# Optimization experiments

Measured on AMD Instinct MI355X. Metric: run time of the kernel, lower is better.

The kernel has to match this reference:

```python
import jax, jax.numpy as jnp
import numpy as np
import itertools

# The repo's eset_ops_4_to_4 builds 69 permutation-equivariant basis ops on a
# rank-4 set tensor x[n, d, i, j, k, l]. We reconstruct the 69-dim basis as all
# order-preserving subset matchings (A, B) with A = kept input index slots,
# B = output slots receiving them (|A| = |B| = s, s = 1..4): sum x over the
# complement of A, then broadcast the reduced tensor into output positions B.
# Count: sum_{s=1..4} C(4,s)^2 = 16 + 36 + 16 + 1 = 69 (Vandermonde C(8,4)=70
# minus the s=0 global-sum term).

def _basis_pairs():
    pairs = []
    for s in range(1, 5):
        for A in itertools.combinations(range(4), s):
            for B in itertools.combinations(range(4), s):
                pairs.append((A, B))
    return pairs  # len == 69

_PAIRS = _basis_pairs()


def _forward(x, coefs, bias):
    # x: (n, d, N, N, N, N); coefs: (d, s_out, 69); bias: (1, s_out, 1,1,1,1)
    out_shape = (x.shape[0], coefs.shape[1]) + x.shape[2:]
    out = jnp.zeros(out_shape, x.dtype)
    for idx, (A, B) in enumerate(_PAIRS):
        sum_axes = tuple(2 + i for i in range(4) if i not in A)
        red = x.sum(axis=sum_axes) if sum_axes else x  # (n, d, N^|A|)
        # mix channels on the SMALL reduced tensor (op and channel mix commute)
        term = jnp.einsum('ds,nd...->ns...', coefs[:, :, idx], red)
        # place kept axes at output slots B (order-preserving), broadcast rest
        for p in range(4):
            if p not in B:
                term = jnp.expand_dims(term, axis=2 + p)
        out = out + term  # broadcasting add == broadcast then accumulate
    return out + bias


def setup_inputs() -> dict:
    key = jax.random.key(0)
    k1, k2 = jax.random.split(key)
    n, d, s_out, N, basis = 2, 8, 8, 32, 69
    x = jax.random.normal(k1, (n, d, N, N, N, N), dtype=jnp.float32)
    std = np.sqrt(2.0 / (d + s_out + basis)).astype(np.float32)
    coefs = std * jax.random.normal(k2, (d, s_out, basis), dtype=jnp.float32)
    bias = jnp.zeros((1, s_out, 1, 1, 1, 1), dtype=jnp.float32)
    return {'x': x, 'coefs': coefs, 'bias': bias}


def reference(x, coefs, bias):
    return _forward(x, coefs, bias)
```

## Files before the change

kernel.cpp:

```cpp
#include <hip/hip_runtime.h>


constexpr size_t R3SZ  = 524288;
constexpr size_t R2SZ  = 16384;
constexpr size_t R1SZ  = 512;
constexpr size_t R3OFF = 0;
constexpr size_t R2OFF = R3OFF + 4 * R3SZ;
constexpr size_t R1OFF = R2OFF + 6 * R2SZ;
constexpr size_t T2OFF = R1OFF + 4 * R1SZ;
constexpr size_t T1OFF = T2OFF + 6 * R2SZ;
constexpr size_t U3OFF = T1OFF + 4 * R1SZ;

__global__ __launch_bounds__(512) void k_red3(const float* __restrict__ x,
                                              float* __restrict__ ws) {
    __shared__ float4 cp[32][4][8];
    __shared__ float  b012[1024];
    __shared__ float4 a2[256];
    const int bid  = blockIdx.x;
    const int t    = threadIdx.x;
    const int half = t >> 8;
    const int tt   = t & 255;
    const int k    = tt >> 3;
    const int l4   = tt & 7;

    if (bid < 512) {
        const int i    = bid & 31;
        const int nd   = bid >> 5;
        const int w4   = (t >> 6) & 3;
        const int lane = t & 63;
        const float* xp = x + ((size_t)nd << 20) + ((size_t)i << 15) + k * 32 + l4 * 4;
        float4 acc = {0.f, 0.f, 0.f, 0.f};
        #pragma unroll
        for (int it = 0; it < 16; ++it) {
            const int j = it * 2 + half;
            float4 v = *(const float4*)(xp + j * 1024);
            acc.x += v.x; acc.y += v.y; acc.z += v.z; acc.w += v.w;
            float h = v.x + v.y + v.z + v.w;
            h += __shfl_xor(h, 1); h += __shfl_xor(h, 2); h += __shfl_xor(h, 4);
            if (l4 == 0) b012[j * 32 + k] = h;
            v.x += __shfl_xor(v.x, 8);  v.y += __shfl_xor(v.y, 8);
            v.z += __shfl_xor(v.z, 8);  v.w += __shfl_xor(v.w, 8);
            v.x += __shfl_xor(v.x, 16); v.y += __shfl_xor(v.y, 16);
            v.z += __shfl_xor(v.z, 16); v.w += __shfl_xor(v.w, 16);
            v.x += __shfl_xor(v.x, 32); v.y += __shfl_xor(v.y, 32);
            v.z += __shfl_xor(v.z, 32); v.w += __shfl_xor(v.w, 32);
            if (lane < 8) cp[j][w4][lane] = v;
        }
        if (half == 1) a2[tt] = acc;
        __syncthreads();
        const size_t base = ((size_t)nd << 15) + ((size_t)i << 10);
        *(float2*)(ws + R3OFF + base + 2 * t) = *(const float2*)(b012 + 2 * t);
        if (half == 0) {
            const int j = tt >> 3, lj = tt & 7;
            float4 s0 = cp[j][0][lj], s1 = cp[j][1][lj];
            float4 s2 = cp[j][2][lj], s3 = cp[j][3][lj];
            float4 s;
            s.x = s0.x + s1.x + s2.x + s3.x;
            s.y = s0.y + s1.y + s2.y + s3.y;
            s.z = s0.z + s1.z + s2.z + s3.z;
            s.w = s0.w + s1.w + s2.w + s3.w;
            *(float4*)(ws + R3OFF + R3SZ + base + j * 32 + lj * 4) = s;
            float4 b = a2[tt];
            acc.x += b.x; acc.y += b.y; acc.z += b.z; acc.w += b.w;
            *(float4*)(ws + R3OFF + 2 * R3SZ + base + k * 32 + l4 * 4) = acc;
        }
    } else {
        const int bb = bid - 512;
        const int j  = bb & 31;
        const int nd = bb >> 5;
        const float* xp = x + ((size_t)nd << 20) + (size_t)j * 1024 + (size_t)tt * 4;
        float4 acc = {0.f, 0.f, 0.f, 0.f};
        #pragma unroll
        for (int it = 0; it < 16; ++it) {
            const int i = it * 2 + half;
            float4 v = *(const float4*)(xp + ((size_t)i << 15));
            acc.x += v.x; acc.y += v.y; acc.z += v.z; acc.w += v.w;
        }
        if (half == 1) a2[tt] = acc;
        __syncthreads();
        if (half == 0) {
            float4 b = a2[tt];
            acc.x += b.x; acc.y += b.y; acc.z += b.z; acc.w += b.w;
            *(float4*)(ws + R3OFF + 3 * R3SZ + ((size_t)nd << 15)
                       + ((size_t)j << 10) + tt * 4) = acc;
        }
    }
}

__global__ __launch_bounds__(256) void k_red21(float* __restrict__ ws) {
    const int gid = blockIdx.x * 256 + threadIdx.x;
    if (gid < 98304) {
        const int b2 = gid >> 14;
        const int r  = gid & 16383;
        const int nd = r >> 10;
        const int p = (r >> 5) & 31, q = r & 31;
        const float* r012 = ws + R3OFF + ((size_t)nd << 15);
        const float* r013 = r012 + R3SZ;
        const float* r023 = r012 + 2 * R3SZ;
        float s = 0.f;
        switch (b2) {
            case 0: { const float* s0 = r012 + p * 1024 + q * 32;
                      for (int m = 0; m < 32; ++m) s += s0[m]; } break;
            case 1: { const float* s0 = r012 + p * 1024 + q;
                      for (int m = 0; m < 32; ++m) s += s0[m * 32]; } break;
            case 2: { const float* s0 = r013 + p * 1024 + q;
                      for (int m = 0; m < 32; ++m) s += s0[m * 32]; } break;
            case 3: { const float* s0 = r012 + p * 32 + q;
                      for (int m = 0; m < 32; ++m) s += s0[m * 1024]; } break;
            case 4: { const float* s0 = r013 + p * 32 + q;
                      for (int m = 0; m < 32; ++m) s += s0[m * 1024]; } break;
            default:{ const float* s0 = r023 + p * 32 + q;
                      for (int m = 0; m < 32; ++m) s += s0[m * 1024]; } break;
        }
        ws[R2OFF + (size_t)b2 * R2SZ + (size_t)nd * 1024 + p * 32 + q] = s;
    } else if (gid < 100352) {
        const int e  = gid - 98304;
        const int b1 = e >> 9;
        const int r  = e & 511;
        const int nd = r >> 5, p = r & 31;
        const float* r012 = ws + R3OFF + ((size_t)nd << 15);
        const float* r013 = r012 + R3SZ;
        float s = 0.f;
        if (b1 == 0)      { const float* s0 = r012 + p * 1024;
                            for (int m = 0; m < 1024; ++m) s += s0[m]; }
        else if (b1 == 1) { const float* s0 = r012 + p * 32;
                            for (int a = 0; a < 32; ++a) for (int m = 0; m < 32; ++m)
                                s += s0[a * 1024 + m]; }
        else if (b1 == 2) { const float* s0 = r012 + p;
                            for (int a = 0; a < 32; ++a) for (int m = 0; m < 32; ++m)
                                s += s0[a * 1024 + m * 32]; }
        else              { const float* s0 = r013 + p;
                            for (int a = 0; a < 32; ++a) for (int m = 0; m < 32; ++m)
                                s += s0[a * 1024 + m * 32]; }
        ws[R1OFF + (size_t)b1 * R1SZ + (size_t)nd * 32 + p] = s;
    }
}

__global__ __launch_bounds__(256) void k_mix21(const float* __restrict__ coefs,
                                               float* __restrict__ ws) {
    __shared__ float cs[4416];
    for (int idx = threadIdx.x; idx < 4416; idx += 256) cs[idx] = coefs[idx];
    __syncthreads();
    const int gid = blockIdx.x * 256 + threadIdx.x;
    if (gid < 98304) {
        const int b2 = gid >> 14;
        const int r  = gid & 16383;
        const int n  = r >> 13;
        const int so = (r >> 10) & 7;
        const int pq = r & 1023;
        float s = 0.f;
        #pragma unroll
        for (int a2 = 0; a2 < 6; ++a2) {
            const float* src = ws + R2OFF + (size_t)a2 * R2SZ + (size_t)(n * 8) * 1024 + pq;
            #pragma unroll
            for (int d = 0; d < 8; ++d)
                s += cs[(d * 8 + so) * 69 + 16 + a2 * 6 + b2] * src[d * 1024];
        }
        ws[T2OFF + (size_t)b2 * R2SZ + (size_t)(n * 8 + so) * 1024 + pq] = s;
    } else if (gid < 100352) {
        const int e  = gid - 98304;
        const int b1 = e >> 9;
        const int r  = e & 511;
        const int n  = r >> 8;
        const int so = (r >> 5) & 7;
        const int p  = r & 31;
        float s = 0.f;
        #pragma unroll
        for (int a1 = 0; a1 < 4; ++a1) {
            const float* src = ws + R1OFF + (size_t)a1 * R1SZ + (size_t)(n * 8) * 32 + p;
            #pragma unroll
            for (int d = 0; d < 8; ++d)
                s += cs[(d * 8 + so) * 69 + a1 * 4 + b1] * src[d * 32];
        }
        ws[T1OFF + (size_t)b1 * R1SZ + (size_t)(n * 8 + so) * 32 + p] = s;
    }
}

__global__ __launch_bounds__(256) void k_mix3(const float* __restrict__ coefs,
                                              const float* __restrict__ bias,
                                              float* __restrict__ ws) {
    __shared__ float cs[4416];
    for (int idx = threadIdx.x; idx < 4416; idx += 256) cs[idx] = coefs[idx];
    __syncthreads();
    const int blk = blockIdx.x;
    const int cb  = blk & 127;
    const int soh = (blk >> 7) & 1;
    const int n   = blk >> 8;
    const int c   = cb * 256 + threadIdx.x;
    const int p1 = c >> 10, p2 = (c >> 5) & 31, p3 = c & 31;
    float v[4][8];
    #pragma unroll
    for (int a = 0; a < 4; ++a)
        #pragma unroll
        for (int d = 0; d < 8; ++d)
            v[a][d] = ws[R3OFF + (size_t)a * R3SZ + (size_t)(n * 8 + d) * 32768 + c];
    const float* T2 = ws + T2OFF;
    const float* T1 = ws + T1OFF;
    #pragma unroll
    for (int b = 0; b < 4; ++b) {
        #pragma unroll
        for (int so2 = 0; so2 < 4; ++so2) {
            const int so = soh * 4 + so2;
            float s = 0.f;
            #pragma unroll
            for (int a = 0; a < 4; ++a)
                #pragma unroll
                for (int d = 0; d < 8; ++d)
                    s += cs[(d * 8 + so) * 69 + 52 + a * 4 + b] * v[a][d];
            const size_t nso = (size_t)(n * 8 + so);
            if (b == 0) {
                s += T2[0 * R2SZ + nso * 1024 + p1 * 32 + p2];
                s += T2[1 * R2SZ + nso * 1024 + p1 * 32 + p3];
                s += T2[3 * R2SZ + nso * 1024 + p2 * 32 + p3];
                s += T1[0 * R1SZ + nso * 32 + p1];
                s += T1[1 * R1SZ + nso * 32 + p2];
                s += T1[2 * R1SZ + nso * 32 + p3];
                s += bias[so];
            } else if (b == 1) {
                s += T2[2 * R2SZ + nso * 1024 + p1 * 32 + p3];
                s += T2[4 * R2SZ + nso * 1024 + p2 * 32 + p3];
                s += T1[3 * R1SZ + nso * 32 + p3];
            } else if (b == 2) {
                s += T2[5 * R2SZ + nso * 1024 + p2 * 32 + p3];
            }
            ws[U3OFF + (size_t)b * R3SZ + nso * 32768 + c] = s;
        }
    }
}

__global__ __launch_bounds__(256) void k_final(const float* __restrict__ x,
                                               const float* __restrict__ coefs,
                                               const float* __restrict__ ws,
                                               float* __restrict__ out) {
    __shared__ float c68[64];
    if (threadIdx.x < 64) c68[threadIdx.x] = coefs[threadIdx.x * 69 + 68];
    __syncthreads();
    const int b = blockIdx.x;
    const int j = b & 31;
    const int i = (b >> 5) & 31;
    const int n = b >> 10;
    const int t = threadIdx.x;
    const int k = t >> 3, lq = t & 7;

    float4 xv[8];
    const float* xb = x + ((size_t)n << 23) + ((size_t)i << 15) + j * 1024 + k * 32 + lq * 4;
    #pragma unroll
    for (int d = 0; d < 8; ++d) xv[d] = *(const float4*)(xb + ((size_t)d << 20));

    const float* U = ws + U3OFF;
    const size_t c012 = (size_t)i * 1024 + j * 32 + k;
    const size_t c013 = (size_t)i * 1024 + j * 32 + lq * 4;
    const size_t c023 = (size_t)i * 1024 + k * 32 + lq * 4;
    const size_t c123 = (size_t)j * 1024 + k * 32 + lq * 4;

    #pragma unroll
    for (int so = 0; so < 8; ++so) {
        const size_t nso = (size_t)(n * 8 + so) << 15;
        const float  u0 = U[0 * R3SZ + nso + c012];
        const float4 u1 = *(const float4*)(U + 1 * R3SZ + nso + c013);
        const float4 u2 = *(const float4*)(U + 2 * R3SZ + nso + c023);
        const float4 u3 = *(const float4*)(U + 3 * R3SZ + nso + c123);
        float4 acc;
        acc.x = u0 + u1.x + u2.x + u3.x;
        acc.y = u0 + u1.y + u2.y + u3.y;
        acc.z = u0 + u1.z + u2.z + u3.z;
        acc.w = u0 + u1.w + u2.w + u3.w;
        #pragma unroll
        for (int d = 0; d < 8; ++d) {
            const float w = c68[d * 8 + so];
            acc.x += w * xv[d].x; acc.y += w * xv[d].y;
            acc.z += w * xv[d].z; acc.w += w * xv[d].w;
        }
        *(float4*)(out + ((size_t)(n * 8 + so) << 20) + ((size_t)i << 15)
                   + j * 1024 + k * 32 + lq * 4) = acc;
    }
}

extern "C" void kernel_launch(void* const* d_in, const int* in_sizes, int n_in,
                              void* d_out, int out_size, void* d_ws, size_t ws_size,
                              hipStream_t stream) {
    const float* x     = (const float*)d_in[0];
    const float* coefs = (const float*)d_in[1];
    const float* bias  = (const float*)d_in[2];
    float* out = (float*)d_out;
    float* ws  = (float*)d_ws;

    hipLaunchKernelGGL(k_red3, dim3(1024), dim3(512), 0, stream, x, ws);
    hipLaunchKernelGGL(k_red21, dim3(392),  dim3(256), 0, stream, ws);
    hipLaunchKernelGGL(k_mix21, dim3(392),  dim3(256), 0, stream, coefs, ws);
    hipLaunchKernelGGL(k_mix3,  dim3(512),  dim3(256), 0, stream, coefs, bias, ws);
    hipLaunchKernelGGL(k_final, dim3(2048), dim3(256), 0, stream, x, coefs, ws, out);
}
```

Before: 190.6 us.

## Fuse rank-2 reductions into red3 epilogue, merge red21/mix21, split mix3 finer

Computes five of the six rank-2 reductions inside the k_red3 epilogue from shared-memory partials, using shuffles and shared-memory sums. The remaining rank-2 and all rank-1 reductions move into a new k_mixT kernel that also does the channel mixing, which removes one launch and the strided global re-reads of the rank-3 workspace. k_mix3 now handles 2 output channels per block instead of 4, doubling its grid. The trade-off is extra __syncthreads and serial per-thread loops in red3, and a small 66-block k_mixT grid that may underfill the GPU.

```diff
diff --git a/kernel.cpp b/kernel.cpp
--- a/kernel.cpp
+++ b/kernel.cpp
@@ -61,8 +61,30 @@
             s.w = s0.w + s1.w + s2.w + s3.w;
             *(float4*)(ws + R3OFF + R3SZ + base + j * 32 + lj * 4) = s;
             float4 b = a2[tt];
+            a2[tt] = s;
             acc.x += b.x; acc.y += b.y; acc.z += b.z; acc.w += b.w;
             *(float4*)(ws + R3OFF + 2 * R3SZ + base + k * 32 + l4 * 4) = acc;
+        }
+        __syncthreads();
+        const size_t r2b = (size_t)nd * 1024 + (size_t)i * 32;
+        if (t < 32) {
+            float s = 0.f;
+            #pragma unroll
+            for (int kk = 0; kk < 32; ++kk) s += b012[t * 32 + ((kk + t) & 31)];
+            ws[R2OFF + 0 * R2SZ + r2b + t] = s;
+        } else if (t < 64) {
+            const int kc = t - 32;
+            float s = 0.f;
+            #pragma unroll
+            for (int j = 0; j < 32; ++j) s += b012[j * 32 + kc];
+            ws[R2OFF + 1 * R2SZ + r2b + kc] = s;
+        } else if (t < 96) {
+            const int l = t - 64;
+            const float* af = (const float*)a2;
+            float s = 0.f;
+            #pragma unroll
+            for (int j = 0; j < 32; ++j) s += af[j * 32 + l];
+            ws[R2OFF + 2 * R2SZ + r2b + l] = s;
         }
     } else {
         const int bb = bid - 512;
@@ -78,101 +100,108 @@
         }
         if (half == 1) a2[tt] = acc;
         __syncthreads();
+        const size_t r2b = (size_t)nd * 1024 + (size_t)j * 32;
         if (half == 0) {
             float4 b = a2[tt];
             acc.x += b.x; acc.y += b.y; acc.z += b.z; acc.w += b.w;
             *(float4*)(ws + R3OFF + 3 * R3SZ + ((size_t)nd << 15)
                        + ((size_t)j << 10) + tt * 4) = acc;
+            float h = acc.x + acc.y + acc.z + acc.w;
+            h += __shfl_xor(h, 1); h += __shfl_xor(h, 2); h += __shfl_xor(h, 4);
+            if ((t & 7) == 0) ws[R2OFF + 3 * R2SZ + r2b + k] = h;
+            float4 c2 = acc;
+            c2.x += __shfl_xor(c2.x, 8);  c2.y += __shfl_xor(c2.y, 8);
+            c2.z += __shfl_xor(c2.z, 8);  c2.w += __shfl_xor(c2.w, 8);
+            c2.x += __shfl_xor(c2.x, 16); c2.y += __shfl_xor(c2.y, 16);
+            c2.z += __shfl_xor(c2.z, 16); c2.w += __shfl_xor(c2.w, 16);
+            c2.x += __shfl_xor(c2.x, 32); c2.y += __shfl_xor(c2.y, 32);
+            c2.z += __shfl_xor(c2.z, 32); c2.w += __shfl_xor(c2.w, 32);
+            if ((t & 63) < 8) cp[0][t >> 6][t & 63] = c2;
+        }
+        __syncthreads();
+        if (t < 8) {
+            float4 s0 = cp[0][0][t], s1 = cp[0][1][t];
+            float4 s2 = cp[0][2][t], s3 = cp[0][3][t];
+            float4 s;
+            s.x = s0.x + s1.x + s2.x + s3.x;
+            s.y = s0.y + s1.y + s2.y + s3.y;
+            s.z = s0.z + s1.z + s2.z + s3.z;
+            s.w = s0.w + s1.w + s2.w + s3.w;
+            *(float4*)(ws + R2OFF + 4 * R2SZ + r2b + t * 4) = s;
         }
     }
 }
 
-__global__ __launch_bounds__(256) void k_red21(float* __restrict__ ws) {
-    const int gid = blockIdx.x * 256 + threadIdx.x;
-    if (gid < 98304) {
-        const int b2 = gid >> 14;
-        const int r  = gid & 16383;
-        const int nd = r >> 10;
-        const int p = (r >> 5) & 31, q = r & 31;
-        const float* r012 = ws + R3OFF + ((size_t)nd << 15);
-        const float* r013 = r012 + R3SZ;
-        const float* r023 = r012 + 2 * R3SZ;
-        float s = 0.f;
-        switch (b2) {
-            case 0: { const float* s0 = r012 + p * 1024 + q * 32;
-                      for (int m = 0; m < 32; ++m) s += s0[m]; } break;
-            case 1: { const float* s0 = r012 + p * 1024 + q;
-                      for (int m = 0; m < 32; ++m) s += s0[m * 32]; } break;
-            case 2: { const float* s0 = r013 + p * 1024 + q;
-                      for (int m = 0; m < 32; ++m) s += s0[m * 32]; } break;
-            case 3: { const float* s0 = r012 + p * 32 + q;
-                      for (int m = 0; m < 32; ++m) s += s0[m * 1024]; } break;
-            case 4: { const float* s0 = r013 + p * 32 + q;
-                      for (int m = 0; m < 32; ++m) s += s0[m * 1024]; } break;
-            default:{ const float* s0 = r023 + p * 32 + q;
-                      for (int m = 0; m < 32; ++m) s += s0[m * 1024]; } break;
-        }
-        ws[R2OFF + (size_t)b2 * R2SZ + (size_t)nd * 1024 + p * 32 + q] = s;
-    } else if (gid < 100352) {
-        const int e  = gid - 98304;
-        const int b1 = e >> 9;
-        const int r  = e & 511;
-        const int nd = r >> 5, p = r & 31;
-        const float* r012 = ws + R3OFF + ((size_t)nd << 15);
-        const float* r013 = r012 + R3SZ;
-        float s = 0.f;
-        if (b1 == 0)      { const float* s0 = r012 + p * 1024;
-                            for (int m = 0; m < 1024; ++m) s += s0[m]; }
-        else if (b1 == 1) { const float* s0 = r012 + p * 32;
-                            for (int a = 0; a < 32; ++a) for (int m = 0; m < 32; ++m)
-                                s += s0[a * 1024 + m]; }
-        else if (b1 == 2) { const float* s0 = r012 + p;
-                            for (int a = 0; a < 32; ++a) for (int m = 0; m < 32; ++m)
-                                s += s0[a * 1024 + m * 32]; }
-        else              { const float* s0 = r013 + p;
-                            for (int a = 0; a < 32; ++a) for (int m = 0; m < 32; ++m)
-                                s += s0[a * 1024 + m * 32]; }
-        ws[R1OFF + (size_t)b1 * R1SZ + (size_t)nd * 32 + p] = s;
-    }
-}
-
-__global__ __launch_bounds__(256) void k_mix21(const float* __restrict__ coefs,
-                                               float* __restrict__ ws) {
+__global__ __launch_bounds__(256) void k_mixT(const float* __restrict__ coefs,
+                                              float* __restrict__ ws) {
     __shared__ float cs[4416];
-    for (int idx = threadIdx.x; idx < 4416; idx += 256) cs[idx] = coefs[idx];
-    __syncthreads();
-    const int gid = blockIdx.x * 256 + threadIdx.x;
-    if (gid < 98304) {
-        const int b2 = gid >> 14;
-        const int r  = gid & 16383;
-        const int n  = r >> 13;
-        const int so = (r >> 10) & 7;
-        const int pq = r & 1023;
-        float s = 0.f;
-        #pragma unroll
-        for (int a2 = 0; a2 < 6; ++a2) {
-            const float* src = ws + R2OFF + (size_t)a2 * R2SZ + (size_t)(n * 8) * 1024 + pq;
+    __shared__ float s23[256];
+    __shared__ float r1[1024];
+    const int tt = threadIdx.x;
+    for (int idx = tt; idx < 4416; idx += 256) cs[idx] = coefs[idx];
+    const int b = blockIdx.x;
+    if (b < 64) {
+        const int n  = b >> 5;
+        const int ch = b & 31;
+        {
+            const int d  = tt >> 5, q0 = tt & 31;
+            const float* r023p = ws + R3OFF + 2 * R3SZ
+                                 + ((size_t)(n * 8 + d) << 15) + ch * 32 + q0;
+            float s = 0.f;
+            #pragma unroll
+            for (int i = 0; i < 32; ++i) s += r023p[i * 1024];
+            s23[d * 32 + q0] = s;
+        }
+        __syncthreads();
+        const int so = tt >> 5, pql = tt & 31;
+        const int pq = ch * 32 + pql;
+        float r2v[5][8];
+        #pragma unroll
+        for (int a2 = 0; a2 < 5; ++a2)
             #pragma unroll
             for (int d = 0; d < 8; ++d)
-                s += cs[(d * 8 + so) * 69 + 16 + a2 * 6 + b2] * src[d * 1024];
-        }
-        ws[T2OFF + (size_t)b2 * R2SZ + (size_t)(n * 8 + so) * 1024 + pq] = s;
-    } else if (gid < 100352) {
-        const int e  = gid - 98304;
-        const int b1 = e >> 9;
-        const int r  = e & 511;
-        const int n  = r >> 8;
-        const int so = (r >> 5) & 7;
-        const int p  = r & 31;
-        float s = 0.f;
-        #pragma unroll
-        for (int a1 = 0; a1 < 4; ++a1) {
-            const float* src = ws + R1OFF + (size_t)a1 * R1SZ + (size_t)(n * 8) * 32 + p;
-            #pragma unroll
-            for (int d = 0; d < 8; ++d)
-                s += cs[(d * 8 + so) * 69 + a1 * 4 + b1] * src[d * 32];
-        }
-        ws[T1OFF + (size_t)b1 * R1SZ + (size_t)(n * 8 + so) * 32 + p] = s;
+                r2v[a2][d] = ws[R2OFF + (size_t)a2 * R2SZ + (size_t)(n * 8 + d) * 1024 + pq];
+        #pragma unroll
+        for (int b2 = 0; b2 < 6; ++b2) {
+            float s = 0.f;
+            #pragma unroll
+            for (int d = 0; d < 8; ++d) {
+                const int cb = (d * 8 + so) * 69 + 16 + b2;
+                #pragma unroll
+                for (int a2 = 0; a2 < 5; ++a2) s += cs[cb + a2 * 6] * r2v[a2][d];
+                s += cs[cb + 30] * s23[d * 32 + pql];
+            }
+            ws[T2OFF + (size_t)b2 * R2SZ + (size_t)(n * 8 + so) * 1024 + pq] = s;
+        }
+    } else {
+        const int n = b - 64;
+        {
+            const int a1 = tt >> 6;
+            const int dd = (tt >> 3) & 7;
+            const int p0 = (tt & 7) * 4;
+            const int src = (a1 == 0) ? 0 : ((a1 == 3) ? 4 : 3);
+            const float* r2a = ws + R2OFF + (size_t)src * R2SZ + (size_t)(n * 8 + dd) * 1024;
+            #pragma unroll
+            for (int pp = 0; pp < 4; ++pp) {
+                const int p = p0 + pp;
+                float s = 0.f;
+                if (a1 <= 1) { for (int q = 0; q < 32; ++q) s += r2a[p * 32 + q]; }
+                else         { for (int q = 0; q < 32; ++q) s += r2a[q * 32 + p]; }
+                r1[(a1 * 8 + dd) * 32 + p] = s;
+            }
+        }
+        __syncthreads();
+        const int so = tt >> 5, p = tt & 31;
+        #pragma unroll
+        for (int b1 = 0; b1 < 4; ++b1) {
+            float s = 0.f;
+            #pragma unroll
+            for (int a1 = 0; a1 < 4; ++a1)
+                #pragma unroll
+                for (int d = 0; d < 8; ++d)
+                    s += cs[(d * 8 + so) * 69 + a1 * 4 + b1] * r1[(a1 * 8 + d) * 32 + p];
+            ws[T1OFF + (size_t)b1 * R1SZ + (size_t)(n * 8 + so) * 32 + p] = s;
+        }
     }
 }
 
@@ -184,8 +213,8 @@
     __syncthreads();
     const int blk = blockIdx.x;
     const int cb  = blk & 127;
-    const int soh = (blk >> 7) & 1;
-    const int n   = blk >> 8;
+    const int sop = (blk >> 7) & 3;
+    const int n   = blk >> 9;
     const int c   = cb * 256 + threadIdx.x;
     const int p1 = c >> 10, p2 = (c >> 5) & 31, p3 = c & 31;
     float v[4][8];
@@ -199,8 +228,8 @@
     #pragma unroll
     for (int b = 0; b < 4; ++b) {
         #pragma unroll
-        for (int so2 = 0; so2 < 4; ++so2) {
-            const int so = soh * 4 + so2;
+        for (int so2 = 0; so2 < 2; ++so2) {
+            const int so = sop * 2 + so2;
             float s = 0.f;
             #pragma unroll
             for (int a = 0; a < 4; ++a)
@@ -286,8 +315,7 @@
     float* ws  = (float*)d_ws;
 
     hipLaunchKernelGGL(k_red3, dim3(1024), dim3(512), 0, stream, x, ws);
-    hipLaunchKernelGGL(k_red21, dim3(392),  dim3(256), 0, stream, ws);
-    hipLaunchKernelGGL(k_mix21, dim3(392),  dim3(256), 0, stream, coefs, ws);
-    hipLaunchKernelGGL(k_mix3,  dim3(512),  dim3(256), 0, stream, coefs, bias, ws);
+    hipLaunchKernelGGL(k_mixT, dim3(66),   dim3(256), 0, stream, coefs, ws);
+    hipLaunchKernelGGL(k_mix3, dim3(1024), dim3(256), 0, stream, coefs, bias, ws);
     hipLaunchKernelGGL(k_final, dim3(2048), dim3(256), 0, stream, x, coefs, ws, out);
 }
```

New measurement: 171.2 us. 1.11x faster.
